# Optimization experiments

Measured on AMD Instinct MI355X. Metric: run time of the kernel, lower is better.

The kernel has to match this reference:

```python
import jax, jax.numpy as jnp
import numpy as np

HID = 1280
CROSS = 2048
HEAD_DIM = 64
N_HEADS = HID // HEAD_DIM  # 20
FF = 4 * HID               # 5120
EPS = 1e-5


def _layernorm(x, g, b):
    mu = jnp.mean(x, axis=-1, keepdims=True)
    var = jnp.mean(jnp.square(x - mu), axis=-1, keepdims=True)
    return (x - mu) * jax.lax.rsqrt(var + EPS) * g + b


def _attention(x_q, x_kv, wq, wk, wv, wo, bo):
    b, t, _ = x_q.shape
    q = x_q @ wq.T  # [b,t,HID]
    k = x_kv @ wk.T
    v = x_kv @ wv.T
    q = q.reshape(b, t, N_HEADS, HEAD_DIM).transpose(0, 2, 1, 3)
    s = x_kv.shape[1]
    k = k.reshape(b, s, N_HEADS, HEAD_DIM).transpose(0, 2, 1, 3)
    v = v.reshape(b, s, N_HEADS, HEAD_DIM).transpose(0, 2, 1, 3)
    scale = HEAD_DIM ** -0.5
    scores = jnp.einsum('bhtd,bhsd->bhts', q, k) * scale
    attn = jax.nn.softmax(scores, axis=-1)
    o = jnp.einsum('bhts,bhsd->bhtd', attn, v)
    o = o.transpose(0, 2, 1, 3).reshape(b, t, HID)
    return o @ wo.T + bo


def setup_inputs() -> dict:
    key = jax.random.key(0)
    ks = jax.random.split(key, 16)
    std = 0.02
    d = {}
    d['x'] = jax.random.normal(ks[0], (2, 2048, HID), jnp.float32)
    d['encoder_hidden_states'] = jax.random.normal(ks[1], (2, 77, CROSS), jnp.float32)
    d['ln1_g'] = jnp.ones((HID,), jnp.float32); d['ln1_b'] = jnp.zeros((HID,), jnp.float32)
    d['ln2_g'] = jnp.ones((HID,), jnp.float32); d['ln2_b'] = jnp.zeros((HID,), jnp.float32)
    d['ln3_g'] = jnp.ones((HID,), jnp.float32); d['ln3_b'] = jnp.zeros((HID,), jnp.float32)
    d['wq1'] = jax.random.normal(ks[2], (HID, HID), jnp.float32) * std
    d['wk1'] = jax.random.normal(ks[3], (HID, HID), jnp.float32) * std
    d['wv1'] = jax.random.normal(ks[4], (HID, HID), jnp.float32) * std
    d['wo1'] = jax.random.normal(ks[5], (HID, HID), jnp.float32) * std
    d['bo1'] = jnp.zeros((HID,), jnp.float32)
    d['wq2'] = jax.random.normal(ks[6], (HID, HID), jnp.float32) * std
    d['wk2'] = jax.random.normal(ks[7], (HID, CROSS), jnp.float32) * std
    d['wv2'] = jax.random.normal(ks[8], (HID, CROSS), jnp.float32) * std
    d['wo2'] = jax.random.normal(ks[9], (HID, HID), jnp.float32) * std
    d['bo2'] = jnp.zeros((HID,), jnp.float32)
    d['w_geglu'] = jax.random.normal(ks[10], (2 * FF, HID), jnp.float32) * std
    d['b_geglu'] = jnp.zeros((2 * FF,), jnp.float32)
    d['w_ffout'] = jax.random.normal(ks[11], (HID, FF), jnp.float32) * std
    d['b_ffout'] = jnp.zeros((HID,), jnp.float32)
    return d


def reference(x, encoder_hidden_states,
              ln1_g, ln1_b, ln2_g, ln2_b, ln3_g, ln3_b,
              wq1, wk1, wv1, wo1, bo1,
              wq2, wk2, wv2, wo2, bo2,
              w_geglu, b_geglu, w_ffout, b_ffout):
    # self-attention
    h = _layernorm(x, ln1_g, ln1_b)
    x = x + _attention(h, h, wq1, wk1, wv1, wo1, bo1)
    # cross-attention
    h = _layernorm(x, ln2_g, ln2_b)
    x = x + _attention(h, encoder_hidden_states, wq2, wk2, wv2, wo2, bo2)
    # GEGLU feed-forward
    h = _layernorm(x, ln3_g, ln3_b)
    proj = h @ w_geglu.T + b_geglu  # [b,t,2*FF]
    x1, x2 = proj[..., :FF], proj[..., FF:]
    ff = (x1 * jax.nn.gelu(x2, approximate=False)) @ w_ffout.T + b_ffout
    return x + ff
```

## Files before the change

### kernel.cpp

```cpp
#include <hip/hip_runtime.h>

typedef unsigned short u16;
typedef __bf16 bf16x8 __attribute__((ext_vector_type(8)));
typedef float f32x4 __attribute__((ext_vector_type(4)));

#define HID 1280
#define NHEADS 20
#define FFD 5120

__device__ __forceinline__ u16 f2b(float f) {
  union { float f; unsigned u; } a; a.f = f;
  unsigned r = a.u + 0x7FFFu + ((a.u >> 16) & 1u);
  return (u16)(r >> 16);
}

__device__ __forceinline__ void g2lds16(const void* g, void* l) {
  __builtin_amdgcn_global_load_lds(
      (__attribute__((address_space(1))) void*)(g),
      (__attribute__((address_space(3))) void*)(l), 16, 0, 0);
}

__device__ __forceinline__ void swz(int& bx, int& by) {
  int nx = gridDim.x, ny = gridDim.y;
  int id = blockIdx.y * nx + blockIdx.x;
  int sx = ((nx & 7) == 0) ? 8 : (((nx & 3) == 0) ? 4 : (((nx & 1) == 0) ? 2 : 1));
  int sy = ((ny & 7) == 0) ? 8 : (((ny & 3) == 0) ? 4 : (((ny & 1) == 0) ? 2 : 1));
  int per = sx * sy;
  int st = id / per, w = id - st * per;
  int nsx = nx / sx;
  int stx = st % nsx, sty = st / nsx;
  bx = stx * sx + (w % sx);
  by = sty * sy + (w / sx);
}

struct CvtArgs {
  const float* src[10];
  u16* dst[10];
  int cum4[11];
};

__global__ __launch_bounds__(256) void cvt_weights(CvtArgs a, int total4) {
  int i = blockIdx.x * 256 + threadIdx.x;
  if (i >= total4) return;
  int seg = 0;
#pragma unroll
  for (int s = 1; s < 10; s++) seg += (i >= a.cum4[s]);
  int j = (i - a.cum4[seg]) * 4;
  float4 f = *(const float4*)(a.src[seg] + j);
  union { unsigned long long u; u16 s[4]; } o;
  o.s[0] = f2b(f.x); o.s[1] = f2b(f.y); o.s[2] = f2b(f.z); o.s[3] = f2b(f.w);
  *(unsigned long long*)(a.dst[seg] + j) = o.u;
}

__global__ __launch_bounds__(256) void cvt_enc(const float* __restrict__ enc,
                                               u16* __restrict__ encp) {
  int i = blockIdx.x * 256 + threadIdx.x;
  int j = i * 4;
  int row = j >> 11;
  unsigned long long out = 0ull;
  if (row < 154) {
    float4 f = *(const float4*)(enc + j);
    union { unsigned long long u; u16 s[4]; } o;
    o.s[0] = f2b(f.x); o.s[1] = f2b(f.y); o.s[2] = f2b(f.z); o.s[3] = f2b(f.w);
    out = o.u;
  }
  *(unsigned long long*)(encp + j) = out;
}

__global__ __launch_bounds__(256) void ln_bf16(const float* __restrict__ X,
                                               const float* __restrict__ g,
                                               const float* __restrict__ bta,
                                               u16* __restrict__ Out) {
  const int row = blockIdx.x, tid = threadIdx.x;
  const float* xr = X + (size_t)row * HID;
  float v[5];
#pragma unroll
  for (int i = 0; i < 5; i++) v[i] = xr[tid + i * 256];
  float s = v[0] + v[1] + v[2] + v[3] + v[4];
#pragma unroll
  for (int off = 32; off >= 1; off >>= 1) s += __shfl_down(s, off);
  __shared__ float red[4];
  if ((tid & 63) == 0) red[tid >> 6] = s;
  __syncthreads();
  float mu = (red[0] + red[1] + red[2] + red[3]) * (1.0f / HID);
  float d = 0.f;
#pragma unroll
  for (int i = 0; i < 5; i++) { float t = v[i] - mu; d += t * t; }
#pragma unroll
  for (int off = 32; off >= 1; off >>= 1) d += __shfl_down(d, off);
  __syncthreads();
  if ((tid & 63) == 0) red[tid >> 6] = d;
  __syncthreads();
  float rstd = rsqrtf((red[0] + red[1] + red[2] + red[3]) * (1.0f / HID) + 1e-5f);
#pragma unroll
  for (int i = 0; i < 5; i++) {
    int c = tid + i * 256;
    Out[(size_t)row * HID + c] = f2b((v[i] - mu) * rstd * g[c] + bta[c]);
  }
}

__global__ __launch_bounds__(256) void gemm_bt(
    const u16* __restrict__ A, const u16* __restrict__ Bw,
    u16* __restrict__ Cb, float* __restrict__ Cf,
    const float* __restrict__ bias, const float* __restrict__ resid,
    int M, int N, int K, int mode, int nsplit) {
  __shared__ u16 As[4096];
  __shared__ u16 Bs[4096];
  const int tid = threadIdx.x;
  const int wid = tid >> 6, lane = tid & 63;
  const int quad = lane >> 4, l16 = lane & 15;
  int bx, by; swz(bx, by);
  const int bm = by * 128, bn = bx * 128;
  const int wm = (wid & 1) * 64, wn = (wid >> 1) * 64;

  const int arow = tid >> 2;
  const int acol = (tid & 3) * 8;
  const u16* Ag0 = A + (size_t)(bm + arow) * K + acol;
  const u16* Ag1 = A + (size_t)(bm + 64 + arow) * K + acol;
  const u16* Bg0 = Bw + (size_t)(bn + arow) * K + acol;
  const u16* Bg1 = Bw + (size_t)(bn + 64 + arow) * K + acol;
  u16* ldsA0 = &As[wid * 512];
  u16* ldsA1 = &As[2048 + wid * 512];
  u16* ldsB0 = &Bs[wid * 512];
  u16* ldsB1 = &Bs[2048 + wid * 512];

  f32x4 acc[4][4] = {};

  for (int k0 = 0; k0 < K; k0 += 32) {
    __syncthreads();
    g2lds16(Ag0 + k0, ldsA0);
    g2lds16(Ag1 + k0, ldsA1);
    g2lds16(Bg0 + k0, ldsB0);
    g2lds16(Bg1 + k0, ldsB1);
    __syncthreads();
    bf16x8 af[4], bfr[4];
#pragma unroll
    for (int mt = 0; mt < 4; mt++)
      af[mt] = *(const bf16x8*)&As[(wm + mt * 16 + l16) * 32 + quad * 8];
#pragma unroll
    for (int nt = 0; nt < 4; nt++)
      bfr[nt] = *(const bf16x8*)&Bs[(wn + nt * 16 + l16) * 32 + quad * 8];
#pragma unroll
    for (int mt = 0; mt < 4; mt++)
#pragma unroll
      for (int nt = 0; nt < 4; nt++)
        acc[mt][nt] = __builtin_amdgcn_mfma_f32_16x16x32_bf16(af[mt], bfr[nt], acc[mt][nt], 0, 0, 0);
  }

  if (mode == 0) {
#pragma unroll
    for (int mt = 0; mt < 4; mt++)
#pragma unroll
      for (int nt = 0; nt < 4; nt++)
#pragma unroll
        for (int r = 0; r < 4; r++) {
          int row = bm + wm + mt * 16 + quad * 4 + r;
          int col = bn + wn + nt * 16 + l16;
          u16 val = f2b(acc[mt][nt][r]);
          if (nsplit > 0) {
            int t = (col >= 2 * nsplit) ? 2 : ((col >= nsplit) ? 1 : 0);
            int dc = col - t * nsplit;
            Cb[(size_t)t * M * nsplit + (size_t)row * nsplit + dc] = val;
          } else {
            Cb[(size_t)row * N + col] = val;
          }
        }
  } else {
#pragma unroll
    for (int mt = 0; mt < 4; mt++)
#pragma unroll
      for (int nt = 0; nt < 4; nt++)
#pragma unroll
        for (int r = 0; r < 4; r++) {
          int row = bm + wm + mt * 16 + quad * 4 + r;
          int col = bn + wn + nt * 16 + l16;
          size_t idx = (size_t)row * N + col;
          Cf[idx] = acc[mt][nt][r] + bias[col] + resid[idx];
        }
  }
}

__global__ __launch_bounds__(256) void gemm_geglu(
    const u16* __restrict__ A, const u16* __restrict__ W,
    const float* __restrict__ bias, u16* __restrict__ Out,
    int M, int K) {
  __shared__ u16 As[4096];
  __shared__ u16 B1s[2048];
  __shared__ u16 B2s[2048];
  const int tid = threadIdx.x;
  const int wid = tid >> 6, lane = tid & 63;
  const int quad = lane >> 4, l16 = lane & 15;
  int bx, by; swz(bx, by);
  const int bm = by * 128, bn = bx * 64;
  const int wm = (wid & 1) * 64, wn = (wid >> 1) * 32;

  const int arow = tid >> 2;
  const int acol = (tid & 3) * 8;
  const u16* Ag0 = A + (size_t)(bm + arow) * K + acol;
  const u16* Ag1 = A + (size_t)(bm + 64 + arow) * K + acol;
  const u16* B1g = W + (size_t)(bn + arow) * K + acol;
  const u16* B2g = W + (size_t)(FFD + bn + arow) * K + acol;

  f32x4 acc1[4][2] = {};
  f32x4 acc2[4][2] = {};

  for (int k0 = 0; k0 < K; k0 += 32) {
    __syncthreads();
    g2lds16(Ag0 + k0, &As[wid * 512]);
    g2lds16(Ag1 + k0, &As[2048 + wid * 512]);
    g2lds16(B1g + k0, &B1s[wid * 512]);
    g2lds16(B2g + k0, &B2s[wid * 512]);
    __syncthreads();
    bf16x8 af[4], b1[2], b2[2];
#pragma unroll
    for (int mt = 0; mt < 4; mt++)
      af[mt] = *(const bf16x8*)&As[(wm + mt * 16 + l16) * 32 + quad * 8];
#pragma unroll
    for (int nt = 0; nt < 2; nt++) {
      b1[nt] = *(const bf16x8*)&B1s[(wn + nt * 16 + l16) * 32 + quad * 8];
      b2[nt] = *(const bf16x8*)&B2s[(wn + nt * 16 + l16) * 32 + quad * 8];
    }
#pragma unroll
    for (int mt = 0; mt < 4; mt++)
#pragma unroll
      for (int nt = 0; nt < 2; nt++) {
        acc1[mt][nt] = __builtin_amdgcn_mfma_f32_16x16x32_bf16(af[mt], b1[nt], acc1[mt][nt], 0, 0, 0);
        acc2[mt][nt] = __builtin_amdgcn_mfma_f32_16x16x32_bf16(af[mt], b2[nt], acc2[mt][nt], 0, 0, 0);
      }
  }

#pragma unroll
  for (int mt = 0; mt < 4; mt++)
#pragma unroll
    for (int nt = 0; nt < 2; nt++)
#pragma unroll
      for (int r = 0; r < 4; r++) {
        int row = bm + wm + mt * 16 + quad * 4 + r;
        int col = bn + wn + nt * 16 + l16;
        float v1 = acc1[mt][nt][r] + bias[col];
        float v2 = acc2[mt][nt][r] + bias[FFD + col];
        float ge = 0.5f * v2 * (1.0f + erff(v2 * 0.70710678118654752440f));
        Out[(size_t)row * FFD + col] = f2b(v1 * ge);
      }
}

#define KSP 72
__global__ __launch_bounds__(256) void flash_attn(
    const u16* __restrict__ Q, const u16* __restrict__ Kb,
    const u16* __restrict__ Vb, u16* __restrict__ O,
    int T, int Sv, float scale) {
  __shared__ u16 Ks[64 * KSP];
  __shared__ u16 Vt[64 * KSP];
  __shared__ u16 Ps[4][16 * KSP];
  const int tid = threadIdx.x, wid = tid >> 6, lane = tid & 63;
  const int quad = lane >> 4, l16 = lane & 15;
  const int b = blockIdx.y / NHEADS, h = blockIdx.y % NHEADS;
  const int q0 = blockIdx.x * 64;

  const size_t qrow = (size_t)(b * T + q0 + wid * 16 + l16);
  bf16x8 aq0 = *(const bf16x8*)&Q[qrow * HID + h * 64 + quad * 8];
  bf16x8 aq1 = *(const bf16x8*)&Q[qrow * HID + h * 64 + 32 + quad * 8];

  f32x4 oacc[4] = {};
  float m_i[4], l_i[4];
#pragma unroll
  for (int r = 0; r < 4; r++) { m_i[r] = -3.0e38f; l_i[r] = 0.f; }

  const int ntiles = (Sv + 63) >> 6;
  for (int t0 = 0; t0 < ntiles; ++t0) {
    __syncthreads();
#pragma unroll
    for (int c = 0; c < 2; ++c) {
      int chunk = c * 256 + tid;
      int srow = chunk >> 3;
      int scol = (chunk & 7) * 8;
      int s = t0 * 64 + srow;
      if (s < Sv) {
        size_t g = (size_t)(b * Sv + s) * HID + h * 64 + scol;
        uint4 kv = *(const uint4*)&Kb[g];
        *(uint4*)&Ks[srow * KSP + scol] = kv;
        union { uint4 u; u16 s[8]; } vv; vv.u = *(const uint4*)&Vb[g];
#pragma unroll
        for (int j = 0; j < 8; j++) Vt[(scol + j) * KSP + srow] = vv.s[j];
      } else {
        uint4 z = make_uint4(0, 0, 0, 0);
        *(uint4*)&Ks[srow * KSP + scol] = z;
#pragma unroll
        for (int j = 0; j < 8; j++) Vt[(scol + j) * KSP + srow] = 0;
      }
    }
    __syncthreads();

    f32x4 sc[4];
#pragma unroll
    for (int nt = 0; nt < 4; nt++) {
      bf16x8 bk0 = *(const bf16x8*)&Ks[(nt * 16 + l16) * KSP + quad * 8];
      bf16x8 bk1 = *(const bf16x8*)&Ks[(nt * 16 + l16) * KSP + 32 + quad * 8];
      f32x4 z = {0.f, 0.f, 0.f, 0.f};
      z = __builtin_amdgcn_mfma_f32_16x16x32_bf16(aq0, bk0, z, 0, 0, 0);
      z = __builtin_amdgcn_mfma_f32_16x16x32_bf16(aq1, bk1, z, 0, 0, 0);
      sc[nt] = z;
    }
    float mnew[4];
#pragma unroll
    for (int r = 0; r < 4; r++) mnew[r] = m_i[r];
#pragma unroll
    for (int nt = 0; nt < 4; nt++) {
      int s = t0 * 64 + nt * 16 + l16;
#pragma unroll
      for (int r = 0; r < 4; r++) {
        float v = (s < Sv) ? sc[nt][r] * scale : -3.0e38f;
        sc[nt][r] = v;
        mnew[r] = fmaxf(mnew[r], v);
      }
    }
#pragma unroll
    for (int off = 8; off >= 1; off >>= 1)
#pragma unroll
      for (int r = 0; r < 4; r++) mnew[r] = fmaxf(mnew[r], __shfl_xor(mnew[r], off));

    float alpha[4], psum[4] = {0, 0, 0, 0};
#pragma unroll
    for (int r = 0; r < 4; r++) alpha[r] = __expf(m_i[r] - mnew[r]);
#pragma unroll
    for (int nt = 0; nt < 4; nt++)
#pragma unroll
      for (int r = 0; r < 4; r++) {
        float p = __expf(sc[nt][r] - mnew[r]);
        sc[nt][r] = p;
        psum[r] += p;
      }
#pragma unroll
    for (int off = 8; off >= 1; off >>= 1)
#pragma unroll
      for (int r = 0; r < 4; r++) psum[r] += __shfl_xor(psum[r], off);
#pragma unroll
    for (int r = 0; r < 4; r++) {
      l_i[r] = l_i[r] * alpha[r] + psum[r];
      m_i[r] = mnew[r];
    }
#pragma unroll
    for (int dt = 0; dt < 4; dt++)
#pragma unroll
      for (int r = 0; r < 4; r++) oacc[dt][r] *= alpha[r];

#pragma unroll
    for (int nt = 0; nt < 4; nt++)
#pragma unroll
      for (int r = 0; r < 4; r++)
        Ps[wid][(quad * 4 + r) * KSP + nt * 16 + l16] = f2b(sc[nt][r]);

    bf16x8 pa0 = *(const bf16x8*)&Ps[wid][l16 * KSP + quad * 8];
    bf16x8 pa1 = *(const bf16x8*)&Ps[wid][l16 * KSP + 32 + quad * 8];

#pragma unroll
    for (int dt = 0; dt < 4; dt++) {
      bf16x8 bv0 = *(const bf16x8*)&Vt[(dt * 16 + l16) * KSP + quad * 8];
      bf16x8 bv1 = *(const bf16x8*)&Vt[(dt * 16 + l16) * KSP + 32 + quad * 8];
      oacc[dt] = __builtin_amdgcn_mfma_f32_16x16x32_bf16(pa0, bv0, oacc[dt], 0, 0, 0);
      oacc[dt] = __builtin_amdgcn_mfma_f32_16x16x32_bf16(pa1, bv1, oacc[dt], 0, 0, 0);
    }
  }

#pragma unroll
  for (int dt = 0; dt < 4; dt++)
#pragma unroll
    for (int r = 0; r < 4; r++) {
      int row = b * T + q0 + wid * 16 + quad * 4 + r;
      int col = h * 64 + dt * 16 + l16;
      O[(size_t)row * HID + col] = f2b(oacc[dt][r] / l_i[r]);
    }
}

extern "C" void kernel_launch(void* const* d_in, const int* in_sizes, int n_in,
                              void* d_out, int out_size, void* d_ws, size_t ws_size,
                              hipStream_t stream) {
  const float* x    = (const float*)d_in[0];
  const float* enc  = (const float*)d_in[1];
  const float* ln1g = (const float*)d_in[2];
  const float* ln1b = (const float*)d_in[3];
  const float* ln2g = (const float*)d_in[4];
  const float* ln2b = (const float*)d_in[5];
  const float* ln3g = (const float*)d_in[6];
  const float* ln3b = (const float*)d_in[7];
  const float* wq1  = (const float*)d_in[8];
  const float* wk1  = (const float*)d_in[9];
  const float* wv1  = (const float*)d_in[10];
  const float* wo1  = (const float*)d_in[11];
  const float* bo1  = (const float*)d_in[12];
  const float* wq2  = (const float*)d_in[13];
  const float* wk2  = (const float*)d_in[14];
  const float* wv2  = (const float*)d_in[15];
  const float* wo2  = (const float*)d_in[16];
  const float* bo2  = (const float*)d_in[17];
  const float* wg   = (const float*)d_in[18];
  const float* bg   = (const float*)d_in[19];
  const float* wf   = (const float*)d_in[20];
  const float* bfo  = (const float*)d_in[21];
  float* out = (float*)d_out;

  const size_t S1 = 1280 * 1280;
  const size_t S2 = 1280 * 2048;
  const size_t SG = 10240 * 1280;
  const size_t SF = 1280 * 5120;
  const size_t ACT = (size_t)4096 * 1280;

  char* ws = (char*)d_ws;
  size_t off = 0;
  auto alloc = [&](size_t bytes) -> void* {
    void* p = ws + off;
    off += (bytes + 255) & ~(size_t)255;
    return p;
  };
  u16* wq1b = (u16*)alloc(S1 * 2);
  u16* wk1b = (u16*)alloc(S1 * 2);
  u16* wv1b = (u16*)alloc(S1 * 2);
  u16* wo1b = (u16*)alloc(S1 * 2);
  u16* wq2b = (u16*)alloc(S1 * 2);
  u16* wk2b = (u16*)alloc(S2 * 2);
  u16* wv2b = (u16*)alloc(S2 * 2);
  u16* wo2b = (u16*)alloc(S1 * 2);
  u16* wgb  = (u16*)alloc(SG * 2);
  u16* wfb  = (u16*)alloc(SF * 2);
  u16* h    = (u16*)alloc(ACT * 2);
  u16* q    = (u16*)alloc(ACT * 2);
  u16* k    = (u16*)alloc(ACT * 2);
  u16* v    = (u16*)alloc(ACT * 2);
  u16* o    = (u16*)alloc(ACT * 2);
  u16* ffin = q;
  u16* k2   = (u16*)alloc((size_t)256 * 1280 * 2);
  u16* v2   = (u16*)alloc((size_t)256 * 1280 * 2);
  u16* encp = (u16*)alloc((size_t)256 * 2048 * 2);
  float* x2 = out;
  float* x3 = (float*)alloc(ACT * 4);
  (void)k; (void)v; (void)ws_size; (void)in_sizes; (void)n_in; (void)out_size;

  CvtArgs ca;
  const float* srcs[10] = {wq1, wk1, wv1, wo1, wq2, wk2, wv2, wo2, wg, wf};
  u16* dsts[10] = {wq1b, wk1b, wv1b, wo1b, wq2b, wk2b, wv2b, wo2b, wgb, wfb};
  int n4s[10] = {(int)(S1/4), (int)(S1/4), (int)(S1/4), (int)(S1/4), (int)(S1/4),
                 (int)(S2/4), (int)(S2/4), (int)(S1/4), (int)(SG/4), (int)(SF/4)};
  ca.cum4[0] = 0;
  for (int i = 0; i < 10; i++) { ca.src[i] = srcs[i]; ca.dst[i] = dsts[i]; ca.cum4[i+1] = ca.cum4[i] + n4s[i]; }
  int total4 = ca.cum4[10];
  cvt_weights<<<(total4 + 255) / 256, 256, 0, stream>>>(ca, total4);
  cvt_enc<<<512, 256, 0, stream>>>(enc, encp);

  ln_bf16<<<4096, 256, 0, stream>>>(x, ln1g, ln1b, h);
  gemm_bt<<<dim3(30, 32), 256, 0, stream>>>(h, wq1b, q, nullptr, nullptr, nullptr,
                                            4096, 3840, 1280, 0, 1280);
  flash_attn<<<dim3(32, 40), 256, 0, stream>>>(q, k, v, o, 2048, 2048, 0.125f);
  gemm_bt<<<dim3(10, 32), 256, 0, stream>>>(o, wo1b, nullptr, x2, bo1, x,
                                            4096, 1280, 1280, 1, 0);
  ln_bf16<<<4096, 256, 0, stream>>>(x2, ln2g, ln2b, h);
  gemm_bt<<<dim3(10, 32), 256, 0, stream>>>(h, wq2b, q, nullptr, nullptr, nullptr,
                                            4096, 1280, 1280, 0, 0);
  gemm_bt<<<dim3(20, 2), 256, 0, stream>>>(encp, wk2b, k2, nullptr, nullptr, nullptr,
                                           256, 2560, 2048, 0, 1280);
  flash_attn<<<dim3(32, 40), 256, 0, stream>>>(q, k2, v2, o, 2048, 77, 0.125f);
  gemm_bt<<<dim3(10, 32), 256, 0, stream>>>(o, wo2b, nullptr, x3, bo2, x2,
                                            4096, 1280, 1280, 1, 0);
  ln_bf16<<<4096, 256, 0, stream>>>(x3, ln3g, ln3b, h);
  gemm_geglu<<<dim3(80, 32), 256, 0, stream>>>(h, wgb, bg, ffin, 4096, 1280);
  gemm_bt<<<dim3(10, 32), 256, 0, stream>>>(ffin, wfb, nullptr, out, bfo, x3,
                                            4096, 1280, 5120, 1, 0);
}
```

Baseline: 956.9 us.

## Swizzle LDS tiles in GEMMs and restructure flash attention with 128-key tiles

The GEMM and GEGLU kernels now XOR-swizzle the 16-byte column chunk on both the global-to-LDS load and the fragment reads, to cut LDS bank conflicts. Flash attention moves to 128-key tiles and loads K straight into swizzled LDS with global_load_lds. It also writes V transposed and P into XOR-swizzled layouts, scales Q once up front, and computes the softmax row sums with an MFMA against a ones vector instead of shuffles. The aim is fewer bank conflicts, fewer barriers per key, and less VALU and shuffle work. The padding checks on K and V loads are gone, so partial tiles such as cross-attention's 77 keys read past the valid rows. Any NaN or Inf read into V there could spread into the output.

```diff
diff --git a/kernel.cpp b/kernel.cpp
--- a/kernel.cpp
+++ b/kernel.cpp
@@ -114,7 +114,7 @@
   const int wm = (wid & 1) * 64, wn = (wid >> 1) * 64;
 
   const int arow = tid >> 2;
-  const int acol = (tid & 3) * 8;
+  const int acol = (((tid & 3) ^ ((tid >> 2) & 3)) * 8);
   const u16* Ag0 = A + (size_t)(bm + arow) * K + acol;
   const u16* Ag1 = A + (size_t)(bm + 64 + arow) * K + acol;
   const u16* Bg0 = Bw + (size_t)(bn + arow) * K + acol;
@@ -125,6 +125,7 @@
   u16* ldsB1 = &Bs[2048 + wid * 512];
 
   f32x4 acc[4][4] = {};
+  const int fsw = (quad ^ (l16 & 3)) * 8;
 
   for (int k0 = 0; k0 < K; k0 += 32) {
     __syncthreads();
@@ -136,10 +137,10 @@
     bf16x8 af[4], bfr[4];
 #pragma unroll
     for (int mt = 0; mt < 4; mt++)
-      af[mt] = *(const bf16x8*)&As[(wm + mt * 16 + l16) * 32 + quad * 8];
+      af[mt] = *(const bf16x8*)&As[(wm + mt * 16 + l16) * 32 + fsw];
 #pragma unroll
     for (int nt = 0; nt < 4; nt++)
-      bfr[nt] = *(const bf16x8*)&Bs[(wn + nt * 16 + l16) * 32 + quad * 8];
+      bfr[nt] = *(const bf16x8*)&Bs[(wn + nt * 16 + l16) * 32 + fsw];
 #pragma unroll
     for (int mt = 0; mt < 4; mt++)
 #pragma unroll
@@ -195,7 +196,7 @@
   const int wm = (wid & 1) * 64, wn = (wid >> 1) * 32;
 
   const int arow = tid >> 2;
-  const int acol = (tid & 3) * 8;
+  const int acol = (((tid & 3) ^ ((tid >> 2) & 3)) * 8);
   const u16* Ag0 = A + (size_t)(bm + arow) * K + acol;
   const u16* Ag1 = A + (size_t)(bm + 64 + arow) * K + acol;
   const u16* B1g = W + (size_t)(bn + arow) * K + acol;
@@ -203,6 +204,7 @@
 
   f32x4 acc1[4][2] = {};
   f32x4 acc2[4][2] = {};
+  const int fsw = (quad ^ (l16 & 3)) * 8;
 
   for (int k0 = 0; k0 < K; k0 += 32) {
     __syncthreads();
@@ -214,11 +216,11 @@
     bf16x8 af[4], b1[2], b2[2];
 #pragma unroll
     for (int mt = 0; mt < 4; mt++)
-      af[mt] = *(const bf16x8*)&As[(wm + mt * 16 + l16) * 32 + quad * 8];
+      af[mt] = *(const bf16x8*)&As[(wm + mt * 16 + l16) * 32 + fsw];
 #pragma unroll
     for (int nt = 0; nt < 2; nt++) {
-      b1[nt] = *(const bf16x8*)&B1s[(wn + nt * 16 + l16) * 32 + quad * 8];
-      b2[nt] = *(const bf16x8*)&B2s[(wn + nt * 16 + l16) * 32 + quad * 8];
+      b1[nt] = *(const bf16x8*)&B1s[(wn + nt * 16 + l16) * 32 + fsw];
+      b2[nt] = *(const bf16x8*)&B2s[(wn + nt * 16 + l16) * 32 + fsw];
     }
 #pragma unroll
     for (int mt = 0; mt < 4; mt++)
@@ -244,14 +246,14 @@
       }
 }
 
-#define KSP 72
+#define BS 128
 __global__ __launch_bounds__(256) void flash_attn(
     const u16* __restrict__ Q, const u16* __restrict__ Kb,
     const u16* __restrict__ Vb, u16* __restrict__ O,
     int T, int Sv, float scale) {
-  __shared__ u16 Ks[64 * KSP];
-  __shared__ u16 Vt[64 * KSP];
-  __shared__ u16 Ps[4][16 * KSP];
+  __shared__ u16 Ks[BS * 64];
+  __shared__ u16 Vt[64 * BS];
+  __shared__ u16 Ps[4][16 * BS];
   const int tid = threadIdx.x, wid = tid >> 6, lane = tid & 63;
   const int quad = lane >> 4, l16 = lane & 15;
   const int b = blockIdx.y / NHEADS, h = blockIdx.y % NHEADS;
@@ -260,83 +262,110 @@
   const size_t qrow = (size_t)(b * T + q0 + wid * 16 + l16);
   bf16x8 aq0 = *(const bf16x8*)&Q[qrow * HID + h * 64 + quad * 8];
   bf16x8 aq1 = *(const bf16x8*)&Q[qrow * HID + h * 64 + 32 + quad * 8];
+#pragma unroll
+  for (int j = 0; j < 8; j++) {
+    aq0[j] = (__bf16)((float)aq0[j] * scale);
+    aq1[j] = (__bf16)((float)aq1[j] * scale);
+  }
+  bf16x8 ones;
+#pragma unroll
+  for (int j = 0; j < 8; j++) ones[j] = (__bf16)1.0f;
 
   f32x4 oacc[4] = {};
   float m_i[4], l_i[4];
 #pragma unroll
-  for (int r = 0; r < 4; r++) { m_i[r] = -3.0e38f; l_i[r] = 0.f; }
-
-  const int ntiles = (Sv + 63) >> 6;
+  for (int r = 0; r < 4; r++) { m_i[r] = -1.0e30f; l_i[r] = 0.f; }
+
+  const int ntiles = (Sv + BS - 1) / BS;
   for (int t0 = 0; t0 < ntiles; ++t0) {
-    __syncthreads();
-#pragma unroll
-    for (int c = 0; c < 2; ++c) {
-      int chunk = c * 256 + tid;
-      int srow = chunk >> 3;
-      int scol = (chunk & 7) * 8;
-      int s = t0 * 64 + srow;
-      if (s < Sv) {
-        size_t g = (size_t)(b * Sv + s) * HID + h * 64 + scol;
-        uint4 kv = *(const uint4*)&Kb[g];
-        *(uint4*)&Ks[srow * KSP + scol] = kv;
-        union { uint4 u; u16 s[8]; } vv; vv.u = *(const uint4*)&Vb[g];
-#pragma unroll
-        for (int j = 0; j < 8; j++) Vt[(scol + j) * KSP + srow] = vv.s[j];
-      } else {
-        uint4 z = make_uint4(0, 0, 0, 0);
-        *(uint4*)&Ks[srow * KSP + scol] = z;
-#pragma unroll
-        for (int j = 0; j < 8; j++) Vt[(scol + j) * KSP + srow] = 0;
-      }
-    }
-    __syncthreads();
-
-    f32x4 sc[4];
-#pragma unroll
-    for (int nt = 0; nt < 4; nt++) {
-      bf16x8 bk0 = *(const bf16x8*)&Ks[(nt * 16 + l16) * KSP + quad * 8];
-      bf16x8 bk1 = *(const bf16x8*)&Ks[(nt * 16 + l16) * KSP + 32 + quad * 8];
+    const int srow0 = b * Sv + t0 * BS;
+    __syncthreads();
+#pragma unroll
+    for (int c = 0; c < 4; ++c) {
+      int slot = c * 256 + tid;
+      int row = slot >> 3, p = slot & 7;
+      int gsrc = p ^ (row & 7);
+      g2lds16(Kb + (size_t)(srow0 + row) * HID + h * 64 + gsrc * 8,
+              &Ks[(size_t)(c * 256 + wid * 64) * 8]);
+    }
+#pragma unroll
+    for (int c = 0; c < 4; ++c) {
+      int slot = c * 256 + tid;
+      int srow = slot >> 3, scol = (slot & 7) * 8;
+      union { uint4 u; u16 e[8]; } vv;
+      vv.u = *(const uint4*)&Vb[(size_t)(srow0 + srow) * HID + h * 64 + scol];
+      int g = srow >> 3, so = srow & 7;
+#pragma unroll
+      for (int j = 0; j < 8; j++) {
+        int d = scol + j;
+        int f = ((d >> 3) ^ d) & 7;
+        Vt[d * BS + ((g ^ f) * 8 + so)] = vv.e[j];
+      }
+    }
+    __syncthreads();
+
+    f32x4 sc[8];
+#pragma unroll
+    for (int nt = 0; nt < 8; nt++) {
+      int s = nt * 16 + l16;
+      int fb = (s & 7) ;
+      bf16x8 bk0 = *(const bf16x8*)&Ks[s * 64 + ((quad ^ fb) * 8)];
+      bf16x8 bk1 = *(const bf16x8*)&Ks[s * 64 + (((quad ^ 4) ^ fb) * 8)];
       f32x4 z = {0.f, 0.f, 0.f, 0.f};
       z = __builtin_amdgcn_mfma_f32_16x16x32_bf16(aq0, bk0, z, 0, 0, 0);
       z = __builtin_amdgcn_mfma_f32_16x16x32_bf16(aq1, bk1, z, 0, 0, 0);
       sc[nt] = z;
     }
+    if ((t0 == ntiles - 1) && (Sv & (BS - 1))) {
+#pragma unroll
+      for (int nt = 0; nt < 8; nt++) {
+        int s = t0 * BS + nt * 16 + l16;
+        if (s >= Sv)
+#pragma unroll
+          for (int r = 0; r < 4; r++) sc[nt][r] = -1.0e30f;
+      }
+    }
     float mnew[4];
 #pragma unroll
     for (int r = 0; r < 4; r++) mnew[r] = m_i[r];
 #pragma unroll
-    for (int nt = 0; nt < 4; nt++) {
-      int s = t0 * 64 + nt * 16 + l16;
+    for (int nt = 0; nt < 8; nt++)
+#pragma unroll
+      for (int r = 0; r < 4; r++) mnew[r] = fmaxf(mnew[r], sc[nt][r]);
+#pragma unroll
+    for (int off = 8; off >= 1; off >>= 1)
+#pragma unroll
+      for (int r = 0; r < 4; r++) mnew[r] = fmaxf(mnew[r], __shfl_xor(mnew[r], off));
+
+    float alpha[4];
+#pragma unroll
+    for (int r = 0; r < 4; r++) alpha[r] = __expf(m_i[r] - mnew[r]);
+#pragma unroll
+    for (int nt = 0; nt < 8; nt++)
+#pragma unroll
+      for (int r = 0; r < 4; r++) sc[nt][r] = __expf(sc[nt][r] - mnew[r]);
+
+#pragma unroll
+    for (int nt = 0; nt < 8; nt++)
 #pragma unroll
       for (int r = 0; r < 4; r++) {
-        float v = (s < Sv) ? sc[nt][r] * scale : -3.0e38f;
-        sc[nt][r] = v;
-        mnew[r] = fmaxf(mnew[r], v);
-      }
-    }
-#pragma unroll
-    for (int off = 8; off >= 1; off >>= 1)
-#pragma unroll
-      for (int r = 0; r < 4; r++) mnew[r] = fmaxf(mnew[r], __shfl_xor(mnew[r], off));
-
-    float alpha[4], psum[4] = {0, 0, 0, 0};
-#pragma unroll
-    for (int r = 0; r < 4; r++) alpha[r] = __expf(m_i[r] - mnew[r]);
-#pragma unroll
-    for (int nt = 0; nt < 4; nt++)
-#pragma unroll
-      for (int r = 0; r < 4; r++) {
-        float p = __expf(sc[nt][r] - mnew[r]);
-        sc[nt][r] = p;
-        psum[r] += p;
-      }
-#pragma unroll
-    for (int off = 8; off >= 1; off >>= 1)
-#pragma unroll
-      for (int r = 0; r < 4; r++) psum[r] += __shfl_xor(psum[r], off);
+        int row = quad * 4 + r, col = nt * 16 + l16;
+        int g = col >> 3;
+        Ps[wid][row * BS + ((g ^ (row & 7)) * 8 + (col & 7))] = f2b(sc[nt][r]);
+      }
+    bf16x8 pa[4];
+#pragma unroll
+    for (int kc = 0; kc < 4; kc++) {
+      int lg = kc * 4 + quad;
+      pa[kc] = *(const bf16x8*)&Ps[wid][l16 * BS + ((lg ^ (l16 & 7)) * 8)];
+    }
+    f32x4 ls = {0.f, 0.f, 0.f, 0.f};
+#pragma unroll
+    for (int kc = 0; kc < 4; kc++)
+      ls = __builtin_amdgcn_mfma_f32_16x16x32_bf16(pa[kc], ones, ls, 0, 0, 0);
 #pragma unroll
     for (int r = 0; r < 4; r++) {
-      l_i[r] = l_i[r] * alpha[r] + psum[r];
+      l_i[r] = l_i[r] * alpha[r] + ls[r];
       m_i[r] = mnew[r];
     }
 #pragma unroll
@@ -345,20 +374,15 @@
       for (int r = 0; r < 4; r++) oacc[dt][r] *= alpha[r];
 
 #pragma unroll
-    for (int nt = 0; nt < 4; nt++)
-#pragma unroll
-      for (int r = 0; r < 4; r++)
-        Ps[wid][(quad * 4 + r) * KSP + nt * 16 + l16] = f2b(sc[nt][r]);
-
-    bf16x8 pa0 = *(const bf16x8*)&Ps[wid][l16 * KSP + quad * 8];
-    bf16x8 pa1 = *(const bf16x8*)&Ps[wid][l16 * KSP + 32 + quad * 8];
-
-#pragma unroll
     for (int dt = 0; dt < 4; dt++) {
-      bf16x8 bv0 = *(const bf16x8*)&Vt[(dt * 16 + l16) * KSP + quad * 8];
-      bf16x8 bv1 = *(const bf16x8*)&Vt[(dt * 16 + l16) * KSP + 32 + quad * 8];
-      oacc[dt] = __builtin_amdgcn_mfma_f32_16x16x32_bf16(pa0, bv0, oacc[dt], 0, 0, 0);
-      oacc[dt] = __builtin_amdgcn_mfma_f32_16x16x32_bf16(pa1, bv1, oacc[dt], 0, 0, 0);
+      int d = dt * 16 + l16;
+      int f = ((d >> 3) ^ d) & 7;
+#pragma unroll
+      for (int kc = 0; kc < 4; kc++) {
+        int lg = kc * 4 + quad;
+        bf16x8 bv = *(const bf16x8*)&Vt[d * BS + ((lg ^ f) * 8)];
+        oacc[dt] = __builtin_amdgcn_mfma_f32_16x16x32_bf16(pa[kc], bv, oacc[dt], 0, 0, 0);
+      }
     }
   }
 
```

New measurement: 884.3 us. 7.6% less time.
